# Performance work log

Measured on AMD Instinct MI355X. Metric: run time of the kernel, lower is better.

## Reference

```python
import jax, jax.numpy as jnp
import numpy as np

MAX_NODES = 8192
MAX_EDGES = 16384
D = 64
NEG = -1e10


def setup_inputs() -> dict:
    key = jax.random.key(0)
    k1, k2, k3, k4, k5, k6 = jax.random.split(key, 6)
    N, E = MAX_NODES, MAX_EDGES
    nodes = jax.random.normal(k1, (N, D), jnp.float32)
    edges = jax.random.normal(k2, (E, D), jnp.float32)
    receivers = jax.random.randint(k3, (E,), 0, N, jnp.int32)
    senders = jax.random.randint(k4, (E,), 0, N, jnp.int32)
    active_nodes = jnp.ones((N,), jnp.float32)
    active_edges = (jnp.arange(E) < E // 4).astype(jnp.float32)  # prefix of active edges
    Wq = jax.random.normal(k5, (D, D), jnp.float32) / jnp.sqrt(jnp.float32(D))
    Wp = jax.random.normal(k6, (D, 1), jnp.float32) * 0.05
    bq = jnp.zeros((D,), jnp.float32)
    bp = jnp.full((1,), -4.0, jnp.float32)
    return dict(nodes=nodes, edges=edges, receivers=receivers, senders=senders,
                active_nodes=active_nodes, active_edges=active_edges,
                Wq=Wq, bq=bq, Wp=Wp, bp=bp)


def _incr_edges(aedges, n):
    # Closed form of n steps of x <- clip(x @ (I + superdiag), 0, 1):
    # out[j] = 1 iff any(aedges[j-n : j+1]) != 0, then last slot forced to 0.
    c = jnp.cumsum(aedges)
    idx = jnp.arange(aedges.shape[0])
    prev = jnp.where(idx - n - 1 >= 0, c[jnp.clip(idx - n - 1, 0)], 0.0)
    out = ((c - prev) > 0).astype(aedges.dtype)
    return out.at[-1].set(0.0)


def reference(nodes, edges, receivers, senders, active_nodes, active_edges, Wq, bq, Wp, bp):
    N, E = MAX_NODES, MAX_EDGES
    key = jax.random.key(42)
    key_prob, key_edges, key_samp = jax.random.split(key, 3)
    nids = jnp.arange(N)
    e_active = active_edges.sum().astype(jnp.int32)

    # 1-2. edge-generation probability per node + Bernoulli sampling of generators
    probs = jax.nn.sigmoid(nodes @ Wp + bp)[:, 0]                       # [N]
    gens = (jax.random.uniform(key_prob, (N,)) < probs * active_nodes).astype(jnp.float32)

    # 3-4. queries and pairwise cosine-similarity scores[i, j] = cos(q_i, h_j)
    queries = nodes @ Wq + bq                                           # [N, D]
    num = queries @ nodes.T                                             # [N, N]
    qn = jnp.sum(queries * queries, -1)                                 # [N]
    hn = jnp.sum(nodes * nodes, -1)                                     # [N]
    scores = num / (jnp.sqrt(qn[:, None] * hn[None, :]) + 1e-8)
    scores = jnp.clip(scores, -10000.0, 10000.0)
    scores = jnp.where(active_nodes[None, :] > 0, scores, NEG)
    gens = gens * (scores.max(-1) > -jnp.inf).astype(jnp.float32)       # threshold = -inf
    scores = jnp.where(jnp.eye(N, dtype=bool), NEG, scores)             # no self-loops

    # 5. sample target j* per generating node (softmax mode)
    select = jnp.where(gens > 0, jax.random.categorical(key_samp, scores, axis=-1), 0)

    # drop generators whose edge (i, j*) already exists
    is_s = nids[:, None] == senders[None, :]                            # [N, E]
    is_r = select[:, None] == receivers[None, :]                        # [N, E]
    exist = jnp.logical_and(is_s, is_r).any(-1) & (gens > 0)
    gens = jnp.where(exist, 0.0, gens)

    # 6. scatter new edges into the fixed-size buffers
    allowed = E - e_active - 1
    n_gens = jnp.clip(gens.astype(jnp.int32).sum(), 0, allowed)
    naedges = _incr_edges(active_edges, n_gens)
    mask_new = naedges * (1.0 - active_edges)                           # [E]
    new_edges = edges + jax.random.normal(key_edges, edges.shape) * mask_new[:, None]

    t1 = (jnp.cumsum(gens) * gens - 1.0).astype(jnp.int32) + (e_active * gens).astype(jnp.int32)
    nsend = jax.ops.segment_sum(nids, t1, E)
    nsend = jnp.where(mask_new > 0, nsend, senders)

    t2 = jnp.cumsum(gens) * gens - gens
    t2 = jnp.where(gens > 0, t2.astype(jnp.int32), -1) + (e_active * gens).astype(jnp.int32)
    nrec = jax.ops.segment_sum(select, t2, E)
    nrec = jnp.where(mask_new > 0, nrec, receivers)

    nrec = jnp.where(naedges > 0, nrec, N - 1)
    nsend = jnp.where(naedges > 0, nsend, N - 1)
    return new_edges, nsend, nrec, naedges
```

## Files before the change

kernel.cpp:

```cpp
#include <hip/hip_runtime.h>
#include <stdint.h>

#define NN 8192
#define NE 16384
#define DD 64
#define GCAP 512
#define SLICES 32
#define NEGV -1e10f
#define TINYF 1.17549435e-38f
#define SQRT2F 1.41421356237f

__device__ __forceinline__ uint2 tf2x32(uint32_t k0, uint32_t k1, uint32_t x0, uint32_t x1) {
  uint32_t ks2 = k0 ^ k1 ^ 0x1BD11BDAu;
  x0 += k0; x1 += k1;
#define TF_R(r) { x0 += x1; x1 = (x1 << (r)) | (x1 >> (32 - (r))); x1 ^= x0; }
  TF_R(13) TF_R(15) TF_R(26) TF_R(6)
  x0 += k1; x1 += ks2 + 1u;
  TF_R(17) TF_R(29) TF_R(16) TF_R(24)
  x0 += ks2; x1 += k0 + 2u;
  TF_R(13) TF_R(15) TF_R(26) TF_R(6)
  x0 += k0; x1 += k1 + 3u;
  TF_R(17) TF_R(29) TF_R(16) TF_R(24)
  x0 += k1; x1 += ks2 + 4u;
  TF_R(13) TF_R(15) TF_R(26) TF_R(6)
  x0 += ks2; x1 += k0 + 5u;
#undef TF_R
  return make_uint2(x0, x1);
}
__device__ __forceinline__ uint2 jax_subkey(uint32_t i) { return tf2x32(0u, 42u, 0u, i); }
__device__ __forceinline__ uint32_t rbits(uint2 k, uint32_t idx) {
  uint2 r = tf2x32(k.x, k.y, 0u, idx);
  return r.x ^ r.y;
}
__device__ __forceinline__ float u01f(uint32_t b) {
  return __uint_as_float((b >> 9) | 0x3F800000u) - 1.0f;
}
__device__ __forceinline__ float erfinv_xla(float x) {
  float w = -log1pf(-x * x);
  float p;
  if (w < 5.0f) {
    w -= 2.5f;
    p = 2.81022636e-08f;
    p = fmaf(p, w, 3.43273939e-07f);
    p = fmaf(p, w, -3.5233877e-06f);
    p = fmaf(p, w, -4.39150654e-06f);
    p = fmaf(p, w, 0.00021858087f);
    p = fmaf(p, w, -0.00125372503f);
    p = fmaf(p, w, -0.00417768164f);
    p = fmaf(p, w, 0.246640727f);
    p = fmaf(p, w, 1.50140941f);
  } else {
    w = sqrtf(w) - 3.0f;
    p = -0.000200214257f;
    p = fmaf(p, w, 0.000100950558f);
    p = fmaf(p, w, 0.00134934322f);
    p = fmaf(p, w, -0.00367342844f);
    p = fmaf(p, w, 0.00573950773f);
    p = fmaf(p, w, -0.0076224613f);
    p = fmaf(p, w, 0.00943887047f);
    p = fmaf(p, w, 1.00167406f);
    p = fmaf(p, w, 2.83297682f);
  }
  return p * x;
}
__device__ __forceinline__ float jax_normal(uint2 k, uint32_t idx) {
  float f = u01f(rbits(k, idx));
  float lo = __uint_as_float(0xBF7FFFFFu);
  float u = fmaxf(lo, f * 2.0f + lo);
  return SQRT2F * erfinv_xla(u);
}
__device__ __forceinline__ float jax_gumbel(uint2 k, uint32_t idx) {
  float f = u01f(rbits(k, idx));
  float u = fmaxf(TINYF, f + TINYF);
  return -logf(-logf(u));
}


__global__ void sg_gens(const float* __restrict__ nodes, const float* __restrict__ Wp,
                        const float* __restrict__ bp, const float* __restrict__ anodes,
                        int* __restrict__ gens0, float* __restrict__ hn) {
  int lane = threadIdx.x & 63;
  int i = blockIdx.x * 4 + (threadIdx.x >> 6);
  float v = nodes[i * DD + lane];
  float ss = v * v;
  float dp = v * Wp[lane];
  for (int off = 32; off > 0; off >>= 1) {
    ss += __shfl_xor(ss, off, 64);
    dp += __shfl_xor(dp, off, 64);
  }
  if (lane == 0) {
    hn[i] = ss;
    float x = dp + bp[0];
    float p = 1.0f / (1.0f + expf(-x));
    uint2 kp = jax_subkey(0u);
    float u = u01f(rbits(kp, (uint32_t)i));
    gens0[i] = (u < p * anodes[i]) ? 1 : 0;
  }
}

__global__ void sg_scan(const float* __restrict__ aedges, const int* __restrict__ gens0,
                        int* __restrict__ c, int* __restrict__ gidx, int* __restrict__ sc) {
  __shared__ int ts[256];
  int t = threadIdx.x;
  int base = t * 64;
  uint64_t bits = 0;
  int s = 0;
  const float4* a4 = (const float4*)(aedges + base);
  for (int k4 = 0; k4 < 16; k4++) {
    float4 v = a4[k4];
    if (v.x != 0.0f) { bits |= 1ull << (4 * k4 + 0); s++; }
    if (v.y != 0.0f) { bits |= 1ull << (4 * k4 + 1); s++; }
    if (v.z != 0.0f) { bits |= 1ull << (4 * k4 + 2); s++; }
    if (v.w != 0.0f) { bits |= 1ull << (4 * k4 + 3); s++; }
  }
  ts[t] = s;
  __syncthreads();
  for (int off = 1; off < 256; off <<= 1) {
    int add = (t >= off) ? ts[t - off] : 0;
    __syncthreads();
    ts[t] += add;
    __syncthreads();
  }
  int run = ts[t] - s;
  for (int k = 0; k < 64; k++) {
    run += (int)((bits >> k) & 1ull);
    c[base + k] = run;
  }
  if (t == 255) { sc[1] = ts[255]; sc[2] = NE - ts[255] - 1; }
  __syncthreads();
  int b2 = t * 32;
  uint32_t gb = 0;
  int s2 = 0;
  const int4* g4 = (const int4*)(gens0 + b2);
  for (int k4 = 0; k4 < 8; k4++) {
    int4 v = g4[k4];
    if (v.x) { gb |= 1u << (4 * k4 + 0); s2++; }
    if (v.y) { gb |= 1u << (4 * k4 + 1); s2++; }
    if (v.z) { gb |= 1u << (4 * k4 + 2); s2++; }
    if (v.w) { gb |= 1u << (4 * k4 + 3); s2++; }
  }
  ts[t] = s2;
  __syncthreads();
  for (int off = 1; off < 256; off <<= 1) {
    int add = (t >= off) ? ts[t - off] : 0;
    __syncthreads();
    ts[t] += add;
    __syncthreads();
  }
  int r = ts[t] - s2;
  for (int k = 0; k < 32; k++)
    if ((gb >> k) & 1u) gidx[r++] = b2 + k;
  if (t == 255) sc[0] = ts[255];
}

__global__ void sg_query(const float* __restrict__ nodes, const float* __restrict__ Wq,
                         const float* __restrict__ bq, const int* __restrict__ gidx,
                         const int* __restrict__ sc, float* __restrict__ qg,
                         float* __restrict__ qnrm) {
  int g = blockIdx.x;
  int G = min(sc[0], GCAP);
  if (g >= G) return;
  int i = gidx[g];
  int t = threadIdx.x;
  const float* nr = nodes + (size_t)i * DD;
  float acc = bq[t];
  for (int k = 0; k < DD; k++) acc = fmaf(nr[k], Wq[k * DD + t], acc);
  qg[g * DD + t] = acc;
  float ss = acc * acc;
  for (int off = 32; off > 0; off >>= 1) ss += __shfl_xor(ss, off, 64);
  if (t == 0) qnrm[g] = ss;
}

__global__ __launch_bounds__(256) void sg_part(
    const float* __restrict__ nodes, const float* __restrict__ anodes,
    const float* __restrict__ hn, const int* __restrict__ gidx,
    const int* __restrict__ sc, const float* __restrict__ qg,
    const float* __restrict__ qnrm, float* __restrict__ party,
    int* __restrict__ partj) {
  __shared__ float sq[4][DD];
  __shared__ float sqn[4];
  __shared__ int si[4];
  __shared__ float wy[4][4];
  __shared__ int wj[4][4];
  int G = min(sc[0], GCAP);
  int nGq = (G + 3) >> 2;
  int total = nGq * SLICES;
  int t = threadIdx.x;
  int wid = t >> 6, lane = t & 63;
  uint2 ks = jax_subkey(2u);
  for (int item = blockIdx.x; item < total; item += gridDim.x) {
    int gq = item >> 5, s = item & 31;
    int g0 = gq * 4;
    if (t < DD) {
      for (int u = 0; u < 4; u++)
        sq[u][t] = (g0 + u < G) ? qg[(g0 + u) * DD + t] : 0.0f;
    }
    if (t < 4) {
      int g = g0 + t;
      si[t] = (g < G) ? gidx[g] : -1;
      sqn[t] = (g < G) ? qnrm[g] : 1.0f;
    }
    __syncthreads();
    int j = s * 256 + t;
    float4 nv[16];
    const float4* np4 = (const float4*)(nodes + (size_t)j * DD);
    for (int k4 = 0; k4 < 16; k4++) nv[k4] = np4[k4];
    float hnj = hn[j];
    float act = anodes[j];
    float yy[4];
    for (int u = 0; u < 4; u++) {
      int iu = si[u];
      if (iu < 0) { yy[u] = -INFINITY; continue; }
      float num = 0.0f;
      for (int k4 = 0; k4 < 16; k4++) {
        const float4 qv = *(const float4*)&sq[u][4 * k4];
        num += nv[k4].x * qv.x + nv[k4].y * qv.y + nv[k4].z * qv.z + nv[k4].w * qv.w;
      }
      float denom = sqrtf(sqn[u] * hnj) + 1e-8f;
      float sco = num / denom;
      sco = fminf(fmaxf(sco, -10000.0f), 10000.0f);
      if (!(act > 0.0f)) sco = NEGV;
      if (j == iu) sco = NEGV;
      yy[u] = sco + jax_gumbel(ks, (uint32_t)iu * (uint32_t)NN + (uint32_t)j);
    }
    for (int u = 0; u < 4; u++) {
      float y = yy[u];
      int bj = j;
      for (int off = 32; off > 0; off >>= 1) {
        float oy = __shfl_xor(y, off, 64);
        int oj = __shfl_xor(bj, off, 64);
        if (oy > y || (oy == y && oj < bj)) { y = oy; bj = oj; }
      }
      if (lane == 0) { wy[u][wid] = y; wj[u][wid] = bj; }
    }
    __syncthreads();
    if (t < 4) {
      int u = t;
      if (g0 + u < G) {
        float y = wy[u][0];
        int bj = wj[u][0];
        for (int w = 1; w < 4; w++) {
          if (wy[u][w] > y || (wy[u][w] == y && wj[u][w] < bj)) { y = wy[u][w]; bj = wj[u][w]; }
        }
        party[(g0 + u) * SLICES + s] = y;
        partj[(g0 + u) * SLICES + s] = bj;
      }
    }
    __syncthreads();
  }
}

__global__ void sg_reduce(const int* __restrict__ sc, const float* __restrict__ party,
                          const int* __restrict__ partj, int* __restrict__ sel,
                          int* __restrict__ keptf) {
  int g = blockIdx.x;
  int G = min(sc[0], GCAP);
  if (g >= G) return;
  int t = threadIdx.x;
  float y = (t < SLICES) ? party[g * SLICES + t] : -INFINITY;
  int bj = (t < SLICES) ? partj[g * SLICES + t] : 0x7fffffff;
  for (int off = 32; off > 0; off >>= 1) {
    float oy = __shfl_xor(y, off, 64);
    int oj = __shfl_xor(bj, off, 64);
    if (oy > y || (oy == y && oj < bj)) { y = oy; bj = oj; }
  }
  if (t == 0) { sel[g] = bj; keptf[g] = 1; }
}

__global__ void sg_exist2(const int* __restrict__ senders, const int* __restrict__ receivers,
                          const int* __restrict__ gidx, const int* __restrict__ sel,
                          const int* __restrict__ sc, int* __restrict__ keptf) {
  __shared__ int lg[GCAP], ls[GCAP];
  int G = min(sc[0], GCAP);
  int t = threadIdx.x;
  for (int g = t; g < G; g += 256) { lg[g] = gidx[g]; ls[g] = sel[g]; }
  __syncthreads();
  int e = blockIdx.x * 256 + t;
  int se = senders[e], re = receivers[e];
  for (int g = 0; g < G; g++)
    if (se == lg[g] && re == ls[g]) keptf[g] = 0;
}

__global__ void sg_rank(const int* __restrict__ gidx, const int* __restrict__ sel,
                        const int* __restrict__ keptf, int* __restrict__ sc,
                        int* __restrict__ fid, int* __restrict__ fsel) {
  __shared__ int ts[256];
  int t = threadIdx.x;
  int G = min(sc[0], GCAP);
  int base = t * 32;
  int s = 0;
  for (int k = 0; k < 32; k++) { int g = base + k; if (g < G) s += keptf[g]; }
  ts[t] = s;
  __syncthreads();
  for (int off = 1; off < 256; off <<= 1) {
    int add = (t >= off) ? ts[t - off] : 0;
    __syncthreads();
    ts[t] += add;
    __syncthreads();
  }
  int r = ts[t] - s;
  for (int k = 0; k < 32; k++) {
    int g = base + k;
    if (g < G && keptf[g]) { fid[r] = gidx[g]; fsel[r] = sel[g]; r++; }
  }
  if (t == 255) {
    int kt = ts[255];
    int allowed = sc[2];
    int ng = kt > 0 ? kt : 0;
    if (ng > allowed) ng = allowed;
    sc[3] = kt; sc[4] = ng;
  }
}

__global__ void sg_mask(const float* __restrict__ aedges, const int* __restrict__ senders,
                        const int* __restrict__ receivers, const int* __restrict__ c,
                        const int* __restrict__ sc, const int* __restrict__ fid,
                        const int* __restrict__ fsel, float* __restrict__ out_send,
                        float* __restrict__ out_rec, float* __restrict__ out_na) {
  int e = blockIdx.x * 256 + threadIdx.x;
  if (e >= NE) return;
  int n = sc[4], ea = sc[1], kept = sc[3];
  int ce = c[e];
  int pidx = e - n - 1;
  int prev = (pidx >= 0) ? c[pidx] : 0;
  int na = ((ce - prev) > 0) ? 1 : 0;
  if (e == NE - 1) na = 0;
  float a = aedges[e];
  float mv = na ? (1.0f - a) : 0.0f;
  float ns, nr;
  if (!na) {
    ns = nr = (float)(NN - 1);
  } else if (mv > 0.0f) {
    int r = e - ea;
    bool ok = (r >= 0 && r < kept);
    ns = ok ? (float)fid[r] : 0.0f;
    nr = ok ? (float)fsel[r] : 0.0f;
  } else {
    ns = (float)senders[e];
    nr = (float)receivers[e];
  }
  out_send[e] = ns;
  out_rec[e] = nr;
  out_na[e] = (float)na;
}

__global__ void sg_edges(const float* __restrict__ edges, const float* __restrict__ aedges,
                         const int* __restrict__ c, const int* __restrict__ sc,
                         float* __restrict__ out_edges) {
  int t4 = blockIdx.x * 256 + threadIdx.x;
  float4 v = ((const float4*)edges)[t4];
  int e = t4 >> 4;
  int n = sc[4];
  int ce = c[e];
  int pidx = e - n - 1;
  int prev = (pidx >= 0) ? c[pidx] : 0;
  int na = ((ce - prev) > 0 && e != NE - 1) ? 1 : 0;
  float mv = na ? (1.0f - aedges[e]) : 0.0f;
  if (mv != 0.0f) {
    uint2 ke = jax_subkey(1u);
    uint32_t base = (uint32_t)t4 * 4u;
    v.x += jax_normal(ke, base + 0u) * mv;
    v.y += jax_normal(ke, base + 1u) * mv;
    v.z += jax_normal(ke, base + 2u) * mv;
    v.w += jax_normal(ke, base + 3u) * mv;
  }
  ((float4*)out_edges)[t4] = v;
}

extern "C" void kernel_launch(void* const* d_in, const int* in_sizes, int n_in,
                              void* d_out, int out_size, void* d_ws, size_t ws_size,
                              hipStream_t stream) {
  const float* nodes     = (const float*)d_in[0];
  const float* edges     = (const float*)d_in[1];
  const int*   receivers = (const int*)d_in[2];
  const int*   senders   = (const int*)d_in[3];
  const float* anodes    = (const float*)d_in[4];
  const float* aedges    = (const float*)d_in[5];
  const float* Wq        = (const float*)d_in[6];
  const float* bq        = (const float*)d_in[7];
  const float* Wp        = (const float*)d_in[8];
  const float* bp        = (const float*)d_in[9];

  float* out       = (float*)d_out;
  float* out_edges = out;
  float* out_send  = out + (size_t)NE * DD;
  float* out_rec   = out_send + NE;
  float* out_na    = out_rec + NE;

  int* sc     = (int*)d_ws;
  int* gens0  = sc + 8;
  int* gidx   = gens0 + NN;
  int* sel    = gidx + NN;
  int* keptf  = sel + GCAP;
  int* fid    = keptf + GCAP;
  int* fsel   = fid + GCAP;
  int* c      = fsel + GCAP;
  int* partj  = c + NE;
  float* hn   = (float*)(partj + GCAP * SLICES);
  float* qg   = hn + NN;
  float* qnrm = qg + GCAP * DD;
  float* party= qnrm + GCAP;

  sg_gens   <<<NN / 4, 256, 0, stream>>>(nodes, Wp, bp, anodes, gens0, hn);
  sg_scan   <<<1, 256, 0, stream>>>(aedges, gens0, c, gidx, sc);
  sg_query  <<<GCAP, 64, 0, stream>>>(nodes, Wq, bq, gidx, sc, qg, qnrm);
  sg_part   <<<4096, 256, 0, stream>>>(nodes, anodes, hn, gidx, sc, qg, qnrm, party, partj);
  sg_reduce <<<GCAP, 64, 0, stream>>>(sc, party, partj, sel, keptf);
  sg_exist2 <<<NE / 256, 256, 0, stream>>>(senders, receivers, gidx, sel, sc, keptf);
  sg_rank   <<<1, 256, 0, stream>>>(gidx, sel, keptf, sc, fid, fsel);
  sg_mask   <<<NE / 256, 256, 0, stream>>>(aedges, senders, receivers, c, sc, fid, fsel,
                                           out_send, out_rec, out_na);
  sg_edges  <<<NE * DD / 4 / 256, 256, 0, stream>>>(edges, aedges, c, sc, out_edges);
}
```

Baseline: 142.9 us.

## Fuse pipeline stages to cut kernel launches from nine to five

Merges the active-edge scan into the gens kernel as an extra block, folds query projection into the partial-argmax kernel, replaces the separate reduce with packed 64-bit atomicMax, fuses exist-check with ranking via a last-block-done counter, and merges mask output into the edge-noise kernel. The goal is to remove launch and inter-kernel serialization overhead on a latency-bound chain. In exchange, the query projection is recomputed for each of the 32 slices, and the design now depends on atomics and a threadfence-based last-block pattern.

Measured after the change: 141.4 us. About the same (-1.0%).

```diff
diff --git a/kernel.cpp b/kernel.cpp
--- a/kernel.cpp
+++ b/kernel.cpp
@@ -74,11 +74,47 @@
   float u = fmaxf(TINYF, f + TINYF);
   return -logf(-logf(u));
 }
-
-
-__global__ void sg_gens(const float* __restrict__ nodes, const float* __restrict__ Wp,
-                        const float* __restrict__ bp, const float* __restrict__ anodes,
-                        int* __restrict__ gens0, float* __restrict__ hn) {
+__device__ __forceinline__ unsigned long long packkey(float y, int j) {
+  uint32_t b = __float_as_uint(y);
+  b = (b & 0x80000000u) ? ~b : (b | 0x80000000u);
+  return ((unsigned long long)b << 32) | (unsigned long long)(0xFFFFFFFFu - (uint32_t)j);
+}
+
+
+__global__ void sg_gens_scan(const float* __restrict__ nodes, const float* __restrict__ Wp,
+                             const float* __restrict__ bp, const float* __restrict__ anodes,
+                             const float* __restrict__ aedges, int* __restrict__ gens0,
+                             float* __restrict__ hn, int* __restrict__ c, int* __restrict__ sc) {
+  if (blockIdx.x >= 2048) {
+    __shared__ int ts[256];
+    int t = threadIdx.x;
+    int base = t * 64;
+    uint64_t bits = 0;
+    int s = 0;
+    const float4* a4 = (const float4*)(aedges + base);
+    for (int k4 = 0; k4 < 16; k4++) {
+      float4 v = a4[k4];
+      if (v.x != 0.0f) { bits |= 1ull << (4 * k4 + 0); s++; }
+      if (v.y != 0.0f) { bits |= 1ull << (4 * k4 + 1); s++; }
+      if (v.z != 0.0f) { bits |= 1ull << (4 * k4 + 2); s++; }
+      if (v.w != 0.0f) { bits |= 1ull << (4 * k4 + 3); s++; }
+    }
+    ts[t] = s;
+    __syncthreads();
+    for (int off = 1; off < 256; off <<= 1) {
+      int add = (t >= off) ? ts[t - off] : 0;
+      __syncthreads();
+      ts[t] += add;
+      __syncthreads();
+    }
+    int run = ts[t] - s;
+    for (int k = 0; k < 64; k++) {
+      run += (int)((bits >> k) & 1ull);
+      c[base + k] = run;
+    }
+    if (t == 255) { sc[1] = ts[255]; sc[2] = NE - ts[255] - 1; }
+    return;
+  }
   int lane = threadIdx.x & 63;
   int i = blockIdx.x * 4 + (threadIdx.x >> 6);
   float v = nodes[i * DD + lane];
@@ -98,36 +134,11 @@
   }
 }
 
-__global__ void sg_scan(const float* __restrict__ aedges, const int* __restrict__ gens0,
-                        int* __restrict__ c, int* __restrict__ gidx, int* __restrict__ sc) {
+__global__ void sg_compact(const int* __restrict__ gens0, int* __restrict__ gidx,
+                           int* __restrict__ sc, int* __restrict__ keptf,
+                           unsigned long long* __restrict__ asel) {
   __shared__ int ts[256];
   int t = threadIdx.x;
-  int base = t * 64;
-  uint64_t bits = 0;
-  int s = 0;
-  const float4* a4 = (const float4*)(aedges + base);
-  for (int k4 = 0; k4 < 16; k4++) {
-    float4 v = a4[k4];
-    if (v.x != 0.0f) { bits |= 1ull << (4 * k4 + 0); s++; }
-    if (v.y != 0.0f) { bits |= 1ull << (4 * k4 + 1); s++; }
-    if (v.z != 0.0f) { bits |= 1ull << (4 * k4 + 2); s++; }
-    if (v.w != 0.0f) { bits |= 1ull << (4 * k4 + 3); s++; }
-  }
-  ts[t] = s;
-  __syncthreads();
-  for (int off = 1; off < 256; off <<= 1) {
-    int add = (t >= off) ? ts[t - off] : 0;
-    __syncthreads();
-    ts[t] += add;
-    __syncthreads();
-  }
-  int run = ts[t] - s;
-  for (int k = 0; k < 64; k++) {
-    run += (int)((bits >> k) & 1ull);
-    c[base + k] = run;
-  }
-  if (t == 255) { sc[1] = ts[255]; sc[2] = NE - ts[255] - 1; }
-  __syncthreads();
   int b2 = t * 32;
   uint32_t gb = 0;
   int s2 = 0;
@@ -140,6 +151,9 @@
     if (v.w) { gb |= 1u << (4 * k4 + 3); s2++; }
   }
   ts[t] = s2;
+  keptf[2 * t] = 1; keptf[2 * t + 1] = 1;
+  asel[2 * t] = 0ull; asel[2 * t + 1] = 0ull;
+  if (t == 0) sc[5] = 0;
   __syncthreads();
   for (int off = 1; off < 256; off <<= 1) {
     int add = (t >= off) ? ts[t - off] : 0;
@@ -153,31 +167,13 @@
   if (t == 255) sc[0] = ts[255];
 }
 
-__global__ void sg_query(const float* __restrict__ nodes, const float* __restrict__ Wq,
-                         const float* __restrict__ bq, const int* __restrict__ gidx,
-                         const int* __restrict__ sc, float* __restrict__ qg,
-                         float* __restrict__ qnrm) {
-  int g = blockIdx.x;
-  int G = min(sc[0], GCAP);
-  if (g >= G) return;
-  int i = gidx[g];
-  int t = threadIdx.x;
-  const float* nr = nodes + (size_t)i * DD;
-  float acc = bq[t];
-  for (int k = 0; k < DD; k++) acc = fmaf(nr[k], Wq[k * DD + t], acc);
-  qg[g * DD + t] = acc;
-  float ss = acc * acc;
-  for (int off = 32; off > 0; off >>= 1) ss += __shfl_xor(ss, off, 64);
-  if (t == 0) qnrm[g] = ss;
-}
-
 __global__ __launch_bounds__(256) void sg_part(
     const float* __restrict__ nodes, const float* __restrict__ anodes,
     const float* __restrict__ hn, const int* __restrict__ gidx,
-    const int* __restrict__ sc, const float* __restrict__ qg,
-    const float* __restrict__ qnrm, float* __restrict__ party,
-    int* __restrict__ partj) {
+    const int* __restrict__ sc, const float* __restrict__ Wq,
+    const float* __restrict__ bq, unsigned long long* __restrict__ asel) {
   __shared__ float sq[4][DD];
+  __shared__ float sn[4][DD];
   __shared__ float sqn[4];
   __shared__ int si[4];
   __shared__ float wy[4][4];
@@ -191,15 +187,21 @@
   for (int item = blockIdx.x; item < total; item += gridDim.x) {
     int gq = item >> 5, s = item & 31;
     int g0 = gq * 4;
-    if (t < DD) {
-      for (int u = 0; u < 4; u++)
-        sq[u][t] = (g0 + u < G) ? qg[(g0 + u) * DD + t] : 0.0f;
-    }
     if (t < 4) {
       int g = g0 + t;
       si[t] = (g < G) ? gidx[g] : -1;
-      sqn[t] = (g < G) ? qnrm[g] : 1.0f;
-    }
+    }
+    __syncthreads();
+    int iu_w = si[wid];
+    sn[wid][lane] = (iu_w >= 0) ? nodes[(size_t)iu_w * DD + lane] : 0.0f;
+    __syncthreads();
+    float q = bq[lane];
+#pragma unroll
+    for (int k = 0; k < DD; k++) q = fmaf(sn[wid][k], Wq[k * DD + lane], q);
+    sq[wid][lane] = q;
+    float ssq = q * q;
+    for (int off = 32; off > 0; off >>= 1) ssq += __shfl_xor(ssq, off, 64);
+    if (lane == 0) sqn[wid] = ssq;
     __syncthreads();
     int j = s * 256 + t;
     float4 nv[16];
@@ -234,62 +236,48 @@
       if (lane == 0) { wy[u][wid] = y; wj[u][wid] = bj; }
     }
     __syncthreads();
-    if (t < 4) {
+    if (t < 4 && g0 + t < G) {
       int u = t;
-      if (g0 + u < G) {
-        float y = wy[u][0];
-        int bj = wj[u][0];
-        for (int w = 1; w < 4; w++) {
-          if (wy[u][w] > y || (wy[u][w] == y && wj[u][w] < bj)) { y = wy[u][w]; bj = wj[u][w]; }
-        }
-        party[(g0 + u) * SLICES + s] = y;
-        partj[(g0 + u) * SLICES + s] = bj;
+      float y = wy[u][0];
+      int bj = wj[u][0];
+      for (int w = 1; w < 4; w++) {
+        if (wy[u][w] > y || (wy[u][w] == y && wj[u][w] < bj)) { y = wy[u][w]; bj = wj[u][w]; }
       }
-    }
-    __syncthreads();
-  }
-}
-
-__global__ void sg_reduce(const int* __restrict__ sc, const float* __restrict__ party,
-                          const int* __restrict__ partj, int* __restrict__ sel,
-                          int* __restrict__ keptf) {
-  int g = blockIdx.x;
-  int G = min(sc[0], GCAP);
-  if (g >= G) return;
-  int t = threadIdx.x;
-  float y = (t < SLICES) ? party[g * SLICES + t] : -INFINITY;
-  int bj = (t < SLICES) ? partj[g * SLICES + t] : 0x7fffffff;
-  for (int off = 32; off > 0; off >>= 1) {
-    float oy = __shfl_xor(y, off, 64);
-    int oj = __shfl_xor(bj, off, 64);
-    if (oy > y || (oy == y && oj < bj)) { y = oy; bj = oj; }
-  }
-  if (t == 0) { sel[g] = bj; keptf[g] = 1; }
-}
-
-__global__ void sg_exist2(const int* __restrict__ senders, const int* __restrict__ receivers,
-                          const int* __restrict__ gidx, const int* __restrict__ sel,
-                          const int* __restrict__ sc, int* __restrict__ keptf) {
+      atomicMax(&asel[g0 + u], packkey(y, bj));
+    }
+    __syncthreads();
+  }
+}
+
+__global__ void sg_exist_rank(const int* __restrict__ senders, const int* __restrict__ receivers,
+                              const int* __restrict__ gidx,
+                              const unsigned long long* __restrict__ asel,
+                              int* __restrict__ sc, int* __restrict__ keptf,
+                              int* __restrict__ fid, int* __restrict__ fsel) {
   __shared__ int lg[GCAP], ls[GCAP];
+  __shared__ int ts[256];
+  __shared__ int lastflag;
   int G = min(sc[0], GCAP);
   int t = threadIdx.x;
-  for (int g = t; g < G; g += 256) { lg[g] = gidx[g]; ls[g] = sel[g]; }
+  for (int g = t; g < G; g += 256) {
+    lg[g] = gidx[g];
+    ls[g] = (int)(0xFFFFFFFFu - (uint32_t)(asel[g] & 0xFFFFFFFFull));
+  }
   __syncthreads();
   int e = blockIdx.x * 256 + t;
   int se = senders[e], re = receivers[e];
   for (int g = 0; g < G; g++)
-    if (se == lg[g] && re == ls[g]) keptf[g] = 0;
-}
-
-__global__ void sg_rank(const int* __restrict__ gidx, const int* __restrict__ sel,
-                        const int* __restrict__ keptf, int* __restrict__ sc,
-                        int* __restrict__ fid, int* __restrict__ fsel) {
-  __shared__ int ts[256];
-  int t = threadIdx.x;
-  int G = min(sc[0], GCAP);
-  int base = t * 32;
-  int s = 0;
-  for (int k = 0; k < 32; k++) { int g = base + k; if (g < G) s += keptf[g]; }
+    if (se == lg[g] && re == ls[g]) atomicAnd(&keptf[g], 0);
+  __threadfence();
+  __syncthreads();
+  if (t == 0) lastflag = (atomicAdd(&sc[5], 1) == (int)gridDim.x - 1);
+  __syncthreads();
+  if (!lastflag) return;
+  __threadfence();
+  int g0i = 2 * t, g1i = 2 * t + 1;
+  int kv0 = (g0i < G) ? atomicAdd(&keptf[g0i], 0) : 0;
+  int kv1 = (g1i < G) ? atomicAdd(&keptf[g1i], 0) : 0;
+  int s = kv0 + kv1;
   ts[t] = s;
   __syncthreads();
   for (int off = 1; off < 256; off <<= 1) {
@@ -299,10 +287,8 @@
     __syncthreads();
   }
   int r = ts[t] - s;
-  for (int k = 0; k < 32; k++) {
-    int g = base + k;
-    if (g < G && keptf[g]) { fid[r] = gidx[g]; fsel[r] = sel[g]; r++; }
-  }
+  if (kv0) { fid[r] = lg[g0i]; fsel[r] = ls[g0i]; r++; }
+  if (kv1) { fid[r] = lg[g1i]; fsel[r] = ls[g1i]; }
   if (t == 255) {
     int kt = ts[255];
     int allowed = sc[2];
@@ -312,42 +298,14 @@
   }
 }
 
-__global__ void sg_mask(const float* __restrict__ aedges, const int* __restrict__ senders,
-                        const int* __restrict__ receivers, const int* __restrict__ c,
-                        const int* __restrict__ sc, const int* __restrict__ fid,
-                        const int* __restrict__ fsel, float* __restrict__ out_send,
-                        float* __restrict__ out_rec, float* __restrict__ out_na) {
-  int e = blockIdx.x * 256 + threadIdx.x;
-  if (e >= NE) return;
-  int n = sc[4], ea = sc[1], kept = sc[3];
-  int ce = c[e];
-  int pidx = e - n - 1;
-  int prev = (pidx >= 0) ? c[pidx] : 0;
-  int na = ((ce - prev) > 0) ? 1 : 0;
-  if (e == NE - 1) na = 0;
-  float a = aedges[e];
-  float mv = na ? (1.0f - a) : 0.0f;
-  float ns, nr;
-  if (!na) {
-    ns = nr = (float)(NN - 1);
-  } else if (mv > 0.0f) {
-    int r = e - ea;
-    bool ok = (r >= 0 && r < kept);
-    ns = ok ? (float)fid[r] : 0.0f;
-    nr = ok ? (float)fsel[r] : 0.0f;
-  } else {
-    ns = (float)senders[e];
-    nr = (float)receivers[e];
-  }
-  out_send[e] = ns;
-  out_rec[e] = nr;
-  out_na[e] = (float)na;
-}
-
-__global__ void sg_edges(const float* __restrict__ edges, const float* __restrict__ aedges,
-                         const int* __restrict__ c, const int* __restrict__ sc,
-                         float* __restrict__ out_edges) {
-  int t4 = blockIdx.x * 256 + threadIdx.x;
+__global__ void sg_out(const float* __restrict__ edges, const float* __restrict__ aedges,
+                       const int* __restrict__ senders, const int* __restrict__ receivers,
+                       const int* __restrict__ c, const int* __restrict__ sc,
+                       const int* __restrict__ fid, const int* __restrict__ fsel,
+                       float* __restrict__ out_edges, float* __restrict__ out_send,
+                       float* __restrict__ out_rec, float* __restrict__ out_na) {
+  int t = threadIdx.x;
+  int t4 = blockIdx.x * 256 + t;
   float4 v = ((const float4*)edges)[t4];
   int e = t4 >> 4;
   int n = sc[4];
@@ -365,6 +323,30 @@
     v.w += jax_normal(ke, base + 3u) * mv;
   }
   ((float4*)out_edges)[t4] = v;
+  if (t < 16) {
+    int ee = blockIdx.x * 16 + t;
+    int ce2 = c[ee];
+    int p2 = ee - n - 1;
+    int prev2 = (p2 >= 0) ? c[p2] : 0;
+    int na2 = ((ce2 - prev2) > 0 && ee != NE - 1) ? 1 : 0;
+    float a2 = aedges[ee];
+    float mv2 = na2 ? (1.0f - a2) : 0.0f;
+    float ns, nr;
+    if (!na2) {
+      ns = nr = (float)(NN - 1);
+    } else if (mv2 > 0.0f) {
+      int r = ee - sc[1];
+      bool ok = (r >= 0 && r < sc[3]);
+      ns = ok ? (float)fid[r] : 0.0f;
+      nr = ok ? (float)fsel[r] : 0.0f;
+    } else {
+      ns = (float)senders[ee];
+      nr = (float)receivers[ee];
+    }
+    out_send[ee] = ns;
+    out_rec[ee] = nr;
+    out_na[ee] = (float)na2;
+  }
 }
 
 extern "C" void kernel_launch(void* const* d_in, const int* in_sizes, int n_in,
@@ -390,25 +372,17 @@
   int* sc     = (int*)d_ws;
   int* gens0  = sc + 8;
   int* gidx   = gens0 + NN;
-  int* sel    = gidx + NN;
-  int* keptf  = sel + GCAP;
+  int* keptf  = gidx + NN;
   int* fid    = keptf + GCAP;
   int* fsel   = fid + GCAP;
   int* c      = fsel + GCAP;
-  int* partj  = c + NE;
-  float* hn   = (float*)(partj + GCAP * SLICES);
-  float* qg   = hn + NN;
-  float* qnrm = qg + GCAP * DD;
-  float* party= qnrm + GCAP;
-
-  sg_gens   <<<NN / 4, 256, 0, stream>>>(nodes, Wp, bp, anodes, gens0, hn);
-  sg_scan   <<<1, 256, 0, stream>>>(aedges, gens0, c, gidx, sc);
-  sg_query  <<<GCAP, 64, 0, stream>>>(nodes, Wq, bq, gidx, sc, qg, qnrm);
-  sg_part   <<<4096, 256, 0, stream>>>(nodes, anodes, hn, gidx, sc, qg, qnrm, party, partj);
-  sg_reduce <<<GCAP, 64, 0, stream>>>(sc, party, partj, sel, keptf);
-  sg_exist2 <<<NE / 256, 256, 0, stream>>>(senders, receivers, gidx, sel, sc, keptf);
-  sg_rank   <<<1, 256, 0, stream>>>(gidx, sel, keptf, sc, fid, fsel);
-  sg_mask   <<<NE / 256, 256, 0, stream>>>(aedges, senders, receivers, c, sc, fid, fsel,
-                                           out_send, out_rec, out_na);
-  sg_edges  <<<NE * DD / 4 / 256, 256, 0, stream>>>(edges, aedges, c, sc, out_edges);
-}
+  unsigned long long* asel = (unsigned long long*)(c + NE);
+  float* hn   = (float*)(asel + GCAP);
+
+  sg_gens_scan  <<<2049, 256, 0, stream>>>(nodes, Wp, bp, anodes, aedges, gens0, hn, c, sc);
+  sg_compact    <<<1, 256, 0, stream>>>(gens0, gidx, sc, keptf, asel);
+  sg_part       <<<4096, 256, 0, stream>>>(nodes, anodes, hn, gidx, sc, Wq, bq, asel);
+  sg_exist_rank <<<NE / 256, 256, 0, stream>>>(senders, receivers, gidx, asel, sc, keptf, fid, fsel);
+  sg_out        <<<NE * DD / 4 / 256, 256, 0, stream>>>(edges, aedges, senders, receivers, c, sc,
+                                                        fid, fsel, out_edges, out_send, out_rec, out_na);
+}
```
